# Kernel tuning notes

Hardware: AMD Instinct MI355X
Metric: run time of the kernel (lower is better)

## Reference

```python
import jax, jax.numpy as jnp
import numpy as np

N, E = 50000, 800000
IN_CH, OUT_CH, HEADS, EDGE_DIM = 128, 32, 4, 16
OUT_TOTAL = OUT_CH * HEADS  # 128 == IN_CH -> skip is Identity
NEG_SLOPE = 0.2
BN_EPS = 1e-5


def setup_inputs() -> dict:
    key = jax.random.key(0)
    ks = jax.random.split(key, 12)
    s = 1.0 / np.sqrt(IN_CH)
    return {
        "x": jax.random.normal(ks[0], (N, IN_CH), jnp.float32),
        "edge_index": jax.random.randint(ks[1], (2, E), 0, N, jnp.int64),
        "edge_attr": jax.random.normal(ks[2], (E, EDGE_DIM), jnp.float32),
        # GATv2Conv params (share_weights=False): lin_l, lin_r, lin_edge, att, bias
        "W_l": jax.random.uniform(ks[3], (IN_CH, OUT_TOTAL), jnp.float32, -s, s),
        "W_r": jax.random.uniform(ks[4], (IN_CH, OUT_TOTAL), jnp.float32, -s, s),
        "W_e": jax.random.uniform(ks[5], (EDGE_DIM, OUT_TOTAL), jnp.float32, -0.25, 0.25),
        "att": jax.random.uniform(ks[6], (HEADS, OUT_CH), jnp.float32, -s, s),
        "bias": jnp.zeros((OUT_TOTAL,), jnp.float32),
        "bn_gamma": jnp.ones((OUT_TOTAL,), jnp.float32),
        "bn_beta": jnp.zeros((OUT_TOTAL,), jnp.float32),
    }


def reference(x, edge_index, edge_attr, W_l, W_r, W_e, att, bias, bn_gamma, bn_beta):
    src, dst = edge_index[0], edge_index[1]
    # GATv2Conv: per-node linear projections, reshaped to [N, H, C]
    xl = (x @ W_l).reshape(N, HEADS, OUT_CH)
    xr = (x @ W_r).reshape(N, HEADS, OUT_CH)
    # edge-wise attention input: x_l[src] + x_r[dst] + lin_edge(edge_attr)
    e = xl[src] + xr[dst] + (edge_attr @ W_e).reshape(E, HEADS, OUT_CH)
    e = jax.nn.leaky_relu(e, NEG_SLOPE)
    score = jnp.einsum('ehc,hc->eh', e, att)  # [E, H]
    # segment softmax over destination nodes
    smax = jax.ops.segment_max(score, dst, num_segments=N)
    ex = jnp.exp(score - smax[dst])
    denom = jax.ops.segment_sum(ex, dst, num_segments=N)
    alpha = ex / denom[dst]  # [E, H]
    # weighted scatter-aggregation of source features
    msg = xl[src] * alpha[:, :, None]  # [E, H, C]
    out = jax.ops.segment_sum(msg, dst, num_segments=N).reshape(N, OUT_TOTAL) + bias
    # BatchNorm1d (training-mode batch stats, biased variance)
    mu = out.mean(axis=0)
    var = out.var(axis=0)
    out = (out - mu) * jax.lax.rsqrt(var + BN_EPS) * bn_gamma + bn_beta
    out = jax.nn.elu(out)
    # dropout: eval -> identity; skip: Identity (in_channels == out_total)
    return out + x
```

## Files before the change

### kernel.cpp

```cpp
#include <hip/hip_runtime.h>
#include <math.h>

#define N_NODES 50000
#define E_EDGES 800000
#define NEG_SLOPE 0.2f
#define BN_EPS 1e-5f
#define NB_SCAN 196
#define NWAVES 8192
#define LDB 132

using bf4 = __attribute__((ext_vector_type(4))) short;
using bf8 = __attribute__((ext_vector_type(8))) short;
using f32x4 = __attribute__((ext_vector_type(4))) float;

__device__ __forceinline__ unsigned short f2b(float f) {
  unsigned u = __float_as_uint(f);
  return (unsigned short)((u + 0x7FFFu + ((u >> 16) & 1u)) >> 16);
}

__global__ __launch_bounds__(256) void k_projm(
    const float* __restrict__ x, const float* __restrict__ Wl,
    const float* __restrict__ Wr, unsigned short* __restrict__ xlb,
    float* __restrict__ xr) {
  __shared__ __align__(16) unsigned short blds[256 * LDB];
  const int t = threadIdx.x;

#pragma unroll
  for (int s = 0; s < 32; ++s) {
    int i4 = s * 256 + t;
    int k = (i4 * 4) >> 8;
    int colb = (i4 * 4) & 255;
    float4 w = (colb < 128) ? *(const float4*)(Wl + k * 128 + colb)
                            : *(const float4*)(Wr + k * 128 + (colb - 128));
    blds[(colb + 0) * LDB + k] = f2b(w.x);
    blds[(colb + 1) * LDB + k] = f2b(w.y);
    blds[(colb + 2) * LDB + k] = f2b(w.z);
    blds[(colb + 3) * LDB + k] = f2b(w.w);
  }
  __syncthreads();

  const int wave = t >> 6, lane = t & 63;
  const int f = lane & 15;
  const int g = lane >> 4;
  const int r0 = blockIdx.x * 64 + wave * 16;
  const int row = r0 + f;
  const bool rok = row < N_NODES;

  f32x4 acc[16];
#pragma unroll
  for (int c = 0; c < 16; ++c) acc[c] = (f32x4){0.f, 0.f, 0.f, 0.f};

#pragma unroll
  for (int ks = 0; ks < 4; ++ks) {
    bf8 a;
    if (rok) {
      const float* ap = x + (size_t)row * 128 + ks * 32 + g * 8;
      float4 a0 = *(const float4*)(ap);
      float4 a1 = *(const float4*)(ap + 4);
      a = (bf8){(short)f2b(a0.x), (short)f2b(a0.y), (short)f2b(a0.z),
                (short)f2b(a0.w), (short)f2b(a1.x), (short)f2b(a1.y),
                (short)f2b(a1.z), (short)f2b(a1.w)};
    } else {
      a = (bf8){0, 0, 0, 0, 0, 0, 0, 0};
    }
#pragma unroll
    for (int c = 0; c < 16; ++c) {
      const bf4* bp =
          (const bf4*)(blds + (c * 16 + f) * LDB + ks * 32 + g * 8);
      bf8 b = __builtin_shufflevector(bp[0], bp[1], 0, 1, 2, 3, 4, 5, 6, 7);
      acc[c] = __builtin_amdgcn_mfma_f32_16x16x32_bf16(a, b, acc[c], 0, 0, 0);
    }
  }

#pragma unroll
  for (int c = 0; c < 16; ++c) {
    int cc = (c * 16 + f) & 127;
#pragma unroll
    for (int r = 0; r < 4; ++r) {
      int rr = r0 + g * 4 + r;
      if (rr < N_NODES) {
        if (c < 8)
          xlb[(size_t)rr * 128 + cc] = f2b(acc[c][r]);
        else
          xr[(size_t)rr * 128 + cc] = acc[c][r];
      }
    }
  }
}

__global__ __launch_bounds__(256) void k_count(const int* __restrict__ ei,
                                               int* __restrict__ deg) {
  int e = blockIdx.x * 256 + threadIdx.x;
  if (e < E_EDGES) atomicAdd(&deg[ei[E_EDGES + e]], 1);
}

__global__ __launch_bounds__(256) void k_scan_blk(const int* __restrict__ deg,
                                                  int* __restrict__ offs,
                                                  int* __restrict__ bsum) {
  __shared__ int s[256];
  int t = threadIdx.x, idx = blockIdx.x * 256 + t;
  int v = (idx < N_NODES) ? deg[idx] : 0;
  s[t] = v;
  __syncthreads();
  int acc = v;
#pragma unroll
  for (int off = 1; off < 256; off <<= 1) {
    int u = (t >= off) ? s[t - off] : 0;
    __syncthreads();
    acc += u;
    s[t] = acc;
    __syncthreads();
  }
  if (idx < N_NODES) offs[idx] = acc - v;
  if (t == 255) bsum[blockIdx.x] = acc;
}

__global__ __launch_bounds__(256) void k_scan_top(int* __restrict__ bsum) {
  __shared__ int s[256];
  int t = threadIdx.x;
  int v = (t < NB_SCAN) ? bsum[t] : 0;
  s[t] = v;
  __syncthreads();
  int acc = v;
#pragma unroll
  for (int off = 1; off < 256; off <<= 1) {
    int u = (t >= off) ? s[t - off] : 0;
    __syncthreads();
    acc += u;
    s[t] = acc;
    __syncthreads();
  }
  if (t < NB_SCAN) bsum[t] = acc - v;
}

__global__ __launch_bounds__(256) void k_scan_add(int* __restrict__ offs,
                                                  const int* __restrict__ bsum) {
  int idx = blockIdx.x * 256 + threadIdx.x;
  if (idx < N_NODES) offs[idx] += bsum[blockIdx.x];
}

__global__ __launch_bounds__(256) void k_fill(const int* __restrict__ ei,
                                              const int* __restrict__ offs,
                                              int* __restrict__ cur,
                                              int2* __restrict__ se) {
  int e = blockIdx.x * 256 + threadIdx.x;
  if (e >= E_EDGES) return;
  int d = ei[E_EDGES + e];
  int p = offs[d] + atomicAdd(&cur[d], 1);
  se[p] = make_int2(ei[e], e);
}

__device__ __forceinline__ float fscore(const float* __restrict__ ea, int e,
                                        const float* we0, const float* we1,
                                        float xrx, float xry, float ax,
                                        float ay, float xlx, float xly) {
  const float4* ea4 = (const float4*)(ea + (size_t)e * 16);
  float xe0 = 0.f, xe1 = 0.f;
#pragma unroll
  for (int k = 0; k < 4; ++k) {
    float4 v = ea4[k];
    xe0 += v.x * we0[4 * k] + v.y * we0[4 * k + 1] + v.z * we0[4 * k + 2] +
           v.w * we0[4 * k + 3];
    xe1 += v.x * we1[4 * k] + v.y * we1[4 * k + 1] + v.z * we1[4 * k + 2] +
           v.w * we1[4 * k + 3];
  }
  float v0 = xlx + xrx + xe0;
  float v1 = xly + xry + xe1;
  v0 = v0 > 0.f ? v0 : NEG_SLOPE * v0;
  v1 = v1 > 0.f ? v1 : NEG_SLOPE * v1;
  float p = v0 * ax + v1 * ay;
  p += __shfl_xor(p, 1);
  p += __shfl_xor(p, 2);
  p += __shfl_xor(p, 4);
  p += __shfl_xor(p, 8);
  return p;
}

#define UPD(p, xx, xy)              \
  {                                 \
    float mn = fmaxf(m, (p));       \
    float sc = __expf(m - mn);      \
    float pe = __expf((p)-mn);      \
    den = den * sc + pe;            \
    a0 = a0 * sc + pe * (xx);       \
    a1 = a1 * sc + pe * (xy);       \
    m = mn;                         \
  }

__global__ __launch_bounds__(256, 8) void k_node(
    const unsigned short* __restrict__ xlb, const float* __restrict__ xr,
    const int2* __restrict__ se, const float* __restrict__ ea,
    const float* __restrict__ We, const float* __restrict__ att,
    const int* __restrict__ offs, const int* __restrict__ deg,
    float* __restrict__ out) {
  const int wid =
      __builtin_amdgcn_readfirstlane((int)((blockIdx.x * 256 + threadIdx.x) >> 6));
  const int lane = threadIdx.x & 63;
  const int c0 = lane * 2;

  float we0[16], we1[16];
#pragma unroll
  for (int k = 0; k < 16; ++k) {
    float2 wv = *(const float2*)(We + k * 128 + c0);
    we0[k] = wv.x;
    we1[k] = wv.y;
  }
  float2 aw = *(const float2*)(att + c0);

  for (int d = wid; d < N_NODES; d += NWAVES) {
    const int base = __builtin_amdgcn_readfirstlane(offs[d]);
    const int n = __builtin_amdgcn_readfirstlane(deg[d]);
    float2 xrd = *(const float2*)(xr + (size_t)d * 128 + c0);

    float m = -INFINITY, den = 0.f, a0 = 0.f, a1 = 0.f;
    int i = 0;
    for (; i + 2 <= n; i += 2) {
      int2 q0 = se[base + i];
      int2 q1 = se[base + i + 1];
      int s0 = __builtin_amdgcn_readfirstlane(q0.x);
      int s1 = __builtin_amdgcn_readfirstlane(q1.x);
      int e0 = __builtin_amdgcn_readfirstlane(q0.y);
      int e1 = __builtin_amdgcn_readfirstlane(q1.y);
      unsigned uA = *(const unsigned*)(xlb + (size_t)s0 * 128 + c0);
      unsigned uB = *(const unsigned*)(xlb + (size_t)s1 * 128 + c0);
      float xAx = __uint_as_float(uA << 16);
      float xAy = __uint_as_float(uA & 0xFFFF0000u);
      float xBx = __uint_as_float(uB << 16);
      float xBy = __uint_as_float(uB & 0xFFFF0000u);
      float pA = fscore(ea, e0, we0, we1, xrd.x, xrd.y, aw.x, aw.y, xAx, xAy);
      float pB = fscore(ea, e1, we0, we1, xrd.x, xrd.y, aw.x, aw.y, xBx, xBy);
      UPD(pA, xAx, xAy);
      UPD(pB, xBx, xBy);
    }
    if (i < n) {
      int2 q = se[base + i];
      int s0 = __builtin_amdgcn_readfirstlane(q.x);
      int e0 = __builtin_amdgcn_readfirstlane(q.y);
      unsigned u = *(const unsigned*)(xlb + (size_t)s0 * 128 + c0);
      float xx = __uint_as_float(u << 16);
      float xy = __uint_as_float(u & 0xFFFF0000u);
      float p = fscore(ea, e0, we0, we1, xrd.x, xrd.y, aw.x, aw.y, xx, xy);
      UPD(p, xx, xy);
    }

    float inv = (n > 0) ? 1.f / den : 0.f;
    float2 o;
    o.x = a0 * inv;
    o.y = a1 * inv;
    *(float2*)(out + (size_t)d * 128 + c0) = o;
  }
}

__global__ __launch_bounds__(256) void k_bnstat(const float* __restrict__ out,
                                                float* __restrict__ bnsum,
                                                float* __restrict__ bnsq) {
  __shared__ float ls[256][4];
  __shared__ float lq[256][4];
  int t = threadIdx.x;
  int cg = t & 31;
  int rg = t >> 5;
  float s0 = 0, s1 = 0, s2 = 0, s3 = 0, q0 = 0, q1 = 0, q2 = 0, q3 = 0;
  for (int r = blockIdx.x * 8 + rg; r < N_NODES; r += gridDim.x * 8) {
    float4 v = ((const float4*)out)[(size_t)r * 32 + cg];
    s0 += v.x; s1 += v.y; s2 += v.z; s3 += v.w;
    q0 += v.x * v.x; q1 += v.y * v.y; q2 += v.z * v.z; q3 += v.w * v.w;
  }
  ls[t][0] = s0; ls[t][1] = s1; ls[t][2] = s2; ls[t][3] = s3;
  lq[t][0] = q0; lq[t][1] = q1; lq[t][2] = q2; lq[t][3] = q3;
  __syncthreads();
  if (t < 32) {
#pragma unroll
    for (int g = 1; g < 8; ++g) {
#pragma unroll
      for (int i = 0; i < 4; ++i) {
        ls[t][i] += ls[g * 32 + t][i];
        lq[t][i] += lq[g * 32 + t][i];
      }
    }
#pragma unroll
    for (int i = 0; i < 4; ++i) {
      unsafeAtomicAdd(bnsum + 4 * t + i, ls[t][i]);
      unsafeAtomicAdd(bnsq + 4 * t + i, lq[t][i]);
    }
  }
}

__global__ void k_bnparam(const float* __restrict__ bnsum,
                          const float* __restrict__ bnsq,
                          const float* __restrict__ gamma,
                          const float* __restrict__ beta,
                          float* __restrict__ scale, float* __restrict__ shift) {
  int j = threadIdx.x;
  float mu = bnsum[j] * (1.0f / N_NODES);
  float var = bnsq[j] * (1.0f / N_NODES) - mu * mu;
  float sc = gamma[j] * rsqrtf(var + BN_EPS);
  scale[j] = sc;
  shift[j] = beta[j] - mu * sc;
}

__global__ __launch_bounds__(256) void k_final(
    const float* __restrict__ agg, const float* __restrict__ x,
    const float* __restrict__ scale, const float* __restrict__ shift,
    float* __restrict__ out) {
  int i4 = blockIdx.x * 256 + threadIdx.x;
  if (i4 >= N_NODES * 128 / 4) return;
  int cbase = (i4 * 4) & 127;
  float4 v = ((const float4*)agg)[i4];
  float4 xv = ((const float4*)x)[i4];
  float4 sc = *(const float4*)(scale + cbase);
  float4 sh = *(const float4*)(shift + cbase);
  float r0 = v.x * sc.x + sh.x;
  float r1 = v.y * sc.y + sh.y;
  float r2 = v.z * sc.z + sh.z;
  float r3 = v.w * sc.w + sh.w;
  r0 = r0 > 0.f ? r0 : expm1f(r0);
  r1 = r1 > 0.f ? r1 : expm1f(r1);
  r2 = r2 > 0.f ? r2 : expm1f(r2);
  r3 = r3 > 0.f ? r3 : expm1f(r3);
  float4 o;
  o.x = r0 + xv.x; o.y = r1 + xv.y; o.z = r2 + xv.z; o.w = r3 + xv.w;
  ((float4*)out)[i4] = o;
}

extern "C" void kernel_launch(void* const* d_in, const int* in_sizes, int n_in,
                              void* d_out, int out_size, void* d_ws,
                              size_t ws_size, hipStream_t stream) {
  const float* x = (const float*)d_in[0];
  const int* ei = (const int*)d_in[1];
  const float* ea = (const float*)d_in[2];
  const float* Wl = (const float*)d_in[3];
  const float* Wr = (const float*)d_in[4];
  const float* We = (const float*)d_in[5];
  const float* att = (const float*)d_in[6];
  const float* gamma = (const float*)d_in[8];
  const float* beta = (const float*)d_in[9];
  float* out = (float*)d_out;

  unsigned short* xlb = (unsigned short*)d_ws;
  float* xr = (float*)(xlb + (size_t)N_NODES * 128);
  int* deg = (int*)(xr + (size_t)N_NODES * 128);
  int* offs = deg + N_NODES;
  int* cur = offs + N_NODES;
  int* bsum = cur + N_NODES;
  int2* se = (int2*)(bsum + 256);
  float* bnsum = (float*)(se + E_EDGES);
  float* bnsq = bnsum + 128;
  float* scale = bnsq + 128;
  float* shift = scale + 128;

  hipMemsetAsync(deg, 0, N_NODES * sizeof(int), stream);
  hipMemsetAsync(cur, 0, N_NODES * sizeof(int), stream);
  hipMemsetAsync(bnsum, 0, 2 * 128 * sizeof(float), stream);

  k_projm<<<(N_NODES + 63) / 64, 256, 0, stream>>>(x, Wl, Wr, xlb, xr);
  k_count<<<(E_EDGES + 255) / 256, 256, 0, stream>>>(ei, deg);
  k_scan_blk<<<NB_SCAN, 256, 0, stream>>>(deg, offs, bsum);
  k_scan_top<<<1, 256, 0, stream>>>(bsum);
  k_scan_add<<<NB_SCAN, 256, 0, stream>>>(offs, bsum);
  k_fill<<<(E_EDGES + 255) / 256, 256, 0, stream>>>(ei, offs, cur, se);
  k_node<<<NWAVES / 4, 256, 0, stream>>>(xlb, xr, se, ea, We, att, offs, deg,
                                         out);
  k_bnstat<<<256, 256, 0, stream>>>(out, bnsum, bnsq);
  k_bnparam<<<1, 128, 0, stream>>>(bnsum, bnsq, gamma, beta, scale, shift);
  k_final<<<(N_NODES * 128 / 4 + 255) / 256, 256, 0, stream>>>(out, x, scale,
                                                               shift, out);
}
```

Before: 282.6 us.

## Pre-sort fp16 edge attributes by destination, store xr in bf16, cut launches

The fill kernel now writes edge attributes in destination-sorted order as packed fp16, so the node kernel reads them contiguously instead of gathering fp32 rows by edge id. It computes the edge projection with fdot2, and xr is stored in bf16. Three memsets are folded into the projection and count kernels, the three-pass scan becomes one single-block kernel, and the BN parameter kernel is merged into the final kernel. This cuts launch count and gather traffic, at the cost of fp16/bf16 precision loss and extra writes in the fill kernel. The single-block serial scan and the zeroing of deg and cur inside k_projm rely on stream ordering before k_count.

After: 341.8 us. +21.0%, slower.

```diff
diff --git a/kernel.cpp b/kernel.cpp
--- a/kernel.cpp
+++ b/kernel.cpp
@@ -5,26 +5,38 @@
 #define E_EDGES 800000
 #define NEG_SLOPE 0.2f
 #define BN_EPS 1e-5f
-#define NB_SCAN 196
 #define NWAVES 8192
 #define LDB 132
+#define SCAN_T 1024
+#define SCAN_C 49
 
 using bf4 = __attribute__((ext_vector_type(4))) short;
 using bf8 = __attribute__((ext_vector_type(8))) short;
 using f32x4 = __attribute__((ext_vector_type(4))) float;
+using half2v = __attribute__((ext_vector_type(2))) _Float16;
 
 __device__ __forceinline__ unsigned short f2b(float f) {
   unsigned u = __float_as_uint(f);
   return (unsigned short)((u + 0x7FFFu + ((u >> 16) & 1u)) >> 16);
 }
+__device__ __forceinline__ float b2f_lo(unsigned u) {
+  return __uint_as_float(u << 16);
+}
+__device__ __forceinline__ float b2f_hi(unsigned u) {
+  return __uint_as_float(u & 0xFFFF0000u);
+}
 
 __global__ __launch_bounds__(256) void k_projm(
     const float* __restrict__ x, const float* __restrict__ Wl,
     const float* __restrict__ Wr, unsigned short* __restrict__ xlb,
-    float* __restrict__ xr) {
+    unsigned short* __restrict__ xrb, int* __restrict__ deg,
+    int* __restrict__ cur) {
+  const int t = threadIdx.x;
+  int gid = blockIdx.x * 256 + t;
+  if (gid < N_NODES) deg[gid] = 0;
+  else if (gid < 2 * N_NODES) cur[gid - N_NODES] = 0;
+
   __shared__ __align__(16) unsigned short blds[256 * LDB];
-  const int t = threadIdx.x;
-
 #pragma unroll
   for (int s = 0; s < 32; ++s) {
     int i4 = s * 256 + t;
@@ -74,95 +86,101 @@
 
 #pragma unroll
   for (int c = 0; c < 16; ++c) {
+    unsigned short* dst = (c < 8) ? xlb : xrb;
     int cc = (c * 16 + f) & 127;
 #pragma unroll
     for (int r = 0; r < 4; ++r) {
       int rr = r0 + g * 4 + r;
-      if (rr < N_NODES) {
-        if (c < 8)
-          xlb[(size_t)rr * 128 + cc] = f2b(acc[c][r]);
-        else
-          xr[(size_t)rr * 128 + cc] = acc[c][r];
-      }
+      if (rr < N_NODES) dst[(size_t)rr * 128 + cc] = f2b(acc[c][r]);
     }
   }
 }
 
 __global__ __launch_bounds__(256) void k_count(const int* __restrict__ ei,
-                                               int* __restrict__ deg) {
-  int e = blockIdx.x * 256 + threadIdx.x;
+                                               int* __restrict__ deg,
+                                               float* __restrict__ bn0) {
+  int t = threadIdx.x;
+  if (blockIdx.x == 0) bn0[t] = 0.f;
+  int e = blockIdx.x * 256 + t;
   if (e < E_EDGES) atomicAdd(&deg[ei[E_EDGES + e]], 1);
 }
 
-__global__ __launch_bounds__(256) void k_scan_blk(const int* __restrict__ deg,
-                                                  int* __restrict__ offs,
-                                                  int* __restrict__ bsum) {
-  __shared__ int s[256];
-  int t = threadIdx.x, idx = blockIdx.x * 256 + t;
-  int v = (idx < N_NODES) ? deg[idx] : 0;
-  s[t] = v;
+__global__ __launch_bounds__(SCAN_T) void k_scan(const int* __restrict__ deg,
+                                                 int* __restrict__ offs) {
+  __shared__ int ts[SCAN_T];
+  int t = threadIdx.x;
+  int base = t * SCAN_C;
+  int sum = 0;
+  for (int k = 0; k < SCAN_C; ++k) {
+    int idx = base + k;
+    if (idx < N_NODES) sum += deg[idx];
+  }
+  ts[t] = sum;
   __syncthreads();
-  int acc = v;
-#pragma unroll
-  for (int off = 1; off < 256; off <<= 1) {
-    int u = (t >= off) ? s[t - off] : 0;
+  int acc = sum;
+  for (int off = 1; off < SCAN_T; off <<= 1) {
+    int u = (t >= off) ? ts[t - off] : 0;
     __syncthreads();
     acc += u;
-    s[t] = acc;
+    ts[t] = acc;
     __syncthreads();
   }
-  if (idx < N_NODES) offs[idx] = acc - v;
-  if (t == 255) bsum[blockIdx.x] = acc;
-}
-
-__global__ __launch_bounds__(256) void k_scan_top(int* __restrict__ bsum) {
-  __shared__ int s[256];
-  int t = threadIdx.x;
-  int v = (t < NB_SCAN) ? bsum[t] : 0;
-  s[t] = v;
-  __syncthreads();
-  int acc = v;
-#pragma unroll
-  for (int off = 1; off < 256; off <<= 1) {
-    int u = (t >= off) ? s[t - off] : 0;
-    __syncthreads();
-    acc += u;
-    s[t] = acc;
-    __syncthreads();
-  }
-  if (t < NB_SCAN) bsum[t] = acc - v;
-}
-
-__global__ __launch_bounds__(256) void k_scan_add(int* __restrict__ offs,
-                                                  const int* __restrict__ bsum) {
-  int idx = blockIdx.x * 256 + threadIdx.x;
-  if (idx < N_NODES) offs[idx] += bsum[blockIdx.x];
+  int run = acc - sum;
+  for (int k = 0; k < SCAN_C; ++k) {
+    int idx = base + k;
+    if (idx < N_NODES) {
+      offs[idx] = run;
+      run += deg[idx];
+    }
+  }
 }
 
 __global__ __launch_bounds__(256) void k_fill(const int* __restrict__ ei,
+                                              const float* __restrict__ ea,
                                               const int* __restrict__ offs,
                                               int* __restrict__ cur,
-                                              int2* __restrict__ se) {
+                                              int* __restrict__ src_s,
+                                              int4* __restrict__ eah) {
   int e = blockIdx.x * 256 + threadIdx.x;
   if (e >= E_EDGES) return;
   int d = ei[E_EDGES + e];
   int p = offs[d] + atomicAdd(&cur[d], 1);
-  se[p] = make_int2(ei[e], e);
-}
-
-__device__ __forceinline__ float fscore(const float* __restrict__ ea, int e,
-                                        const float* we0, const float* we1,
-                                        float xrx, float xry, float ax,
-                                        float ay, float xlx, float xly) {
-  const float4* ea4 = (const float4*)(ea + (size_t)e * 16);
+  src_s[p] = ei[e];
+  const float4* r = (const float4*)(ea + (size_t)e * 16);
+  float4 v0 = r[0], v1 = r[1], v2 = r[2], v3 = r[3];
+  union {
+    half2v h[8];
+    int4 q[2];
+  } u;
+  u.h[0] = (half2v){(_Float16)v0.x, (_Float16)v0.y};
+  u.h[1] = (half2v){(_Float16)v0.z, (_Float16)v0.w};
+  u.h[2] = (half2v){(_Float16)v1.x, (_Float16)v1.y};
+  u.h[3] = (half2v){(_Float16)v1.z, (_Float16)v1.w};
+  u.h[4] = (half2v){(_Float16)v2.x, (_Float16)v2.y};
+  u.h[5] = (half2v){(_Float16)v2.z, (_Float16)v2.w};
+  u.h[6] = (half2v){(_Float16)v3.x, (_Float16)v3.y};
+  u.h[7] = (half2v){(_Float16)v3.z, (_Float16)v3.w};
+  eah[(size_t)p * 2] = u.q[0];
+  eah[(size_t)p * 2 + 1] = u.q[1];
+}
+
+__device__ __forceinline__ float fscore16(const half2v* eav,
+                                          const half2v* we0h,
+                                          const half2v* we1h, float xrx,
+                                          float xry, float ax, float ay,
+                                          float xlx, float xly) {
   float xe0 = 0.f, xe1 = 0.f;
 #pragma unroll
-  for (int k = 0; k < 4; ++k) {
-    float4 v = ea4[k];
-    xe0 += v.x * we0[4 * k] + v.y * we0[4 * k + 1] + v.z * we0[4 * k + 2] +
-           v.w * we0[4 * k + 3];
-    xe1 += v.x * we1[4 * k] + v.y * we1[4 * k + 1] + v.z * we1[4 * k + 2] +
-           v.w * we1[4 * k + 3];
+  for (int k = 0; k < 8; ++k) {
+#if __has_builtin(__builtin_amdgcn_fdot2)
+    xe0 = __builtin_amdgcn_fdot2(eav[k], we0h[k], xe0, false);
+    xe1 = __builtin_amdgcn_fdot2(eav[k], we1h[k], xe1, false);
+#else
+    xe0 += (float)eav[k][0] * (float)we0h[k][0] +
+           (float)eav[k][1] * (float)we0h[k][1];
+    xe1 += (float)eav[k][0] * (float)we1h[k][0] +
+           (float)eav[k][1] * (float)we1h[k][1];
+#endif
   }
   float v0 = xlx + xrx + xe0;
   float v1 = xly + xry + xe1;
@@ -188,58 +206,67 @@
   }
 
 __global__ __launch_bounds__(256, 8) void k_node(
-    const unsigned short* __restrict__ xlb, const float* __restrict__ xr,
-    const int2* __restrict__ se, const float* __restrict__ ea,
-    const float* __restrict__ We, const float* __restrict__ att,
-    const int* __restrict__ offs, const int* __restrict__ deg,
-    float* __restrict__ out) {
-  const int wid =
-      __builtin_amdgcn_readfirstlane((int)((blockIdx.x * 256 + threadIdx.x) >> 6));
+    const unsigned short* __restrict__ xlb,
+    const unsigned short* __restrict__ xrb, const int* __restrict__ src_s,
+    const int4* __restrict__ eah, const float* __restrict__ We,
+    const float* __restrict__ att, const int* __restrict__ offs,
+    const int* __restrict__ deg, float* __restrict__ out) {
+  const int wid = __builtin_amdgcn_readfirstlane(
+      (int)((blockIdx.x * 256 + threadIdx.x) >> 6));
   const int lane = threadIdx.x & 63;
   const int c0 = lane * 2;
 
-  float we0[16], we1[16];
-#pragma unroll
-  for (int k = 0; k < 16; ++k) {
-    float2 wv = *(const float2*)(We + k * 128 + c0);
-    we0[k] = wv.x;
-    we1[k] = wv.y;
+  half2v we0h[8], we1h[8];
+#pragma unroll
+  for (int j = 0; j < 8; ++j) {
+    float2 wa = *(const float2*)(We + (2 * j) * 128 + c0);
+    float2 wb = *(const float2*)(We + (2 * j + 1) * 128 + c0);
+    we0h[j] = (half2v){(_Float16)wa.x, (_Float16)wb.x};
+    we1h[j] = (half2v){(_Float16)wa.y, (_Float16)wb.y};
   }
   float2 aw = *(const float2*)(att + c0);
 
   for (int d = wid; d < N_NODES; d += NWAVES) {
     const int base = __builtin_amdgcn_readfirstlane(offs[d]);
     const int n = __builtin_amdgcn_readfirstlane(deg[d]);
-    float2 xrd = *(const float2*)(xr + (size_t)d * 128 + c0);
+    unsigned ur = *(const unsigned*)(xrb + (size_t)d * 128 + c0);
+    float xrx = b2f_lo(ur), xry = b2f_hi(ur);
 
     float m = -INFINITY, den = 0.f, a0 = 0.f, a1 = 0.f;
     int i = 0;
     for (; i + 2 <= n; i += 2) {
-      int2 q0 = se[base + i];
-      int2 q1 = se[base + i + 1];
-      int s0 = __builtin_amdgcn_readfirstlane(q0.x);
-      int s1 = __builtin_amdgcn_readfirstlane(q1.x);
-      int e0 = __builtin_amdgcn_readfirstlane(q0.y);
-      int e1 = __builtin_amdgcn_readfirstlane(q1.y);
+      int s0 = __builtin_amdgcn_readfirstlane(src_s[base + i]);
+      int s1 = __builtin_amdgcn_readfirstlane(src_s[base + i + 1]);
+      union {
+        int4 q[4];
+        half2v h[16];
+      } u;
+      u.q[0] = eah[(size_t)(base + i) * 2];
+      u.q[1] = eah[(size_t)(base + i) * 2 + 1];
+      u.q[2] = eah[(size_t)(base + i) * 2 + 2];
+      u.q[3] = eah[(size_t)(base + i) * 2 + 3];
       unsigned uA = *(const unsigned*)(xlb + (size_t)s0 * 128 + c0);
       unsigned uB = *(const unsigned*)(xlb + (size_t)s1 * 128 + c0);
-      float xAx = __uint_as_float(uA << 16);
-      float xAy = __uint_as_float(uA & 0xFFFF0000u);
-      float xBx = __uint_as_float(uB << 16);
-      float xBy = __uint_as_float(uB & 0xFFFF0000u);
-      float pA = fscore(ea, e0, we0, we1, xrd.x, xrd.y, aw.x, aw.y, xAx, xAy);
-      float pB = fscore(ea, e1, we0, we1, xrd.x, xrd.y, aw.x, aw.y, xBx, xBy);
+      float xAx = b2f_lo(uA), xAy = b2f_hi(uA);
+      float xBx = b2f_lo(uB), xBy = b2f_hi(uB);
+      float pA =
+          fscore16(u.h, we0h, we1h, xrx, xry, aw.x, aw.y, xAx, xAy);
+      float pB =
+          fscore16(u.h + 8, we0h, we1h, xrx, xry, aw.x, aw.y, xBx, xBy);
       UPD(pA, xAx, xAy);
       UPD(pB, xBx, xBy);
     }
     if (i < n) {
-      int2 q = se[base + i];
-      int s0 = __builtin_amdgcn_readfirstlane(q.x);
-      int e0 = __builtin_amdgcn_readfirstlane(q.y);
-      unsigned u = *(const unsigned*)(xlb + (size_t)s0 * 128 + c0);
-      float xx = __uint_as_float(u << 16);
-      float xy = __uint_as_float(u & 0xFFFF0000u);
-      float p = fscore(ea, e0, we0, we1, xrd.x, xrd.y, aw.x, aw.y, xx, xy);
+      int s0 = __builtin_amdgcn_readfirstlane(src_s[base + i]);
+      union {
+        int4 q[2];
+        half2v h[8];
+      } u;
+      u.q[0] = eah[(size_t)(base + i) * 2];
+      u.q[1] = eah[(size_t)(base + i) * 2 + 1];
+      unsigned uv = *(const unsigned*)(xlb + (size_t)s0 * 128 + c0);
+      float xx = b2f_lo(uv), xy = b2f_hi(uv);
+      float p = fscore16(u.h, we0h, we1h, xrx, xry, aw.x, aw.y, xx, xy);
       UPD(p, xx, xy);
     }
 
@@ -285,30 +312,29 @@
   }
 }
 
-__global__ void k_bnparam(const float* __restrict__ bnsum,
-                          const float* __restrict__ bnsq,
-                          const float* __restrict__ gamma,
-                          const float* __restrict__ beta,
-                          float* __restrict__ scale, float* __restrict__ shift) {
-  int j = threadIdx.x;
-  float mu = bnsum[j] * (1.0f / N_NODES);
-  float var = bnsq[j] * (1.0f / N_NODES) - mu * mu;
-  float sc = gamma[j] * rsqrtf(var + BN_EPS);
-  scale[j] = sc;
-  shift[j] = beta[j] - mu * sc;
-}
-
 __global__ __launch_bounds__(256) void k_final(
     const float* __restrict__ agg, const float* __restrict__ x,
-    const float* __restrict__ scale, const float* __restrict__ shift,
+    const float* __restrict__ bnsum, const float* __restrict__ bnsq,
+    const float* __restrict__ gamma, const float* __restrict__ beta,
     float* __restrict__ out) {
-  int i4 = blockIdx.x * 256 + threadIdx.x;
-  if (i4 >= N_NODES * 128 / 4) return;
+  __shared__ __align__(16) float ssc[128];
+  __shared__ __align__(16) float ssh[128];
+  int t = threadIdx.x;
+  if (t < 128) {
+    float mu = bnsum[t] * (1.0f / N_NODES);
+    float var = bnsq[t] * (1.0f / N_NODES) - mu * mu;
+    float sc = gamma[t] * rsqrtf(var + BN_EPS);
+    ssc[t] = sc;
+    ssh[t] = beta[t] - mu * sc;
+  }
+  __syncthreads();
+  int i4 = blockIdx.x * 256 + t;
+  if (i4 >= N_NODES * 32) return;
   int cbase = (i4 * 4) & 127;
   float4 v = ((const float4*)agg)[i4];
   float4 xv = ((const float4*)x)[i4];
-  float4 sc = *(const float4*)(scale + cbase);
-  float4 sh = *(const float4*)(shift + cbase);
+  float4 sc = *(const float4*)(ssc + cbase);
+  float4 sh = *(const float4*)(ssh + cbase);
   float r0 = v.x * sc.x + sh.x;
   float r1 = v.y * sc.y + sh.y;
   float r2 = v.z * sc.z + sh.z;
@@ -337,31 +363,24 @@
   float* out = (float*)d_out;
 
   unsigned short* xlb = (unsigned short*)d_ws;
-  float* xr = (float*)(xlb + (size_t)N_NODES * 128);
-  int* deg = (int*)(xr + (size_t)N_NODES * 128);
+  unsigned short* xrb = xlb + (size_t)N_NODES * 128;
+  int* deg = (int*)(xrb + (size_t)N_NODES * 128);
   int* offs = deg + N_NODES;
   int* cur = offs + N_NODES;
-  int* bsum = cur + N_NODES;
-  int2* se = (int2*)(bsum + 256);
-  float* bnsum = (float*)(se + E_EDGES);
+  int* src_s = cur + N_NODES;
+  int4* eah = (int4*)(src_s + E_EDGES);
+  float* bnsum = (float*)(eah + (size_t)E_EDGES * 2);
   float* bnsq = bnsum + 128;
-  float* scale = bnsq + 128;
-  float* shift = scale + 128;
-
-  hipMemsetAsync(deg, 0, N_NODES * sizeof(int), stream);
-  hipMemsetAsync(cur, 0, N_NODES * sizeof(int), stream);
-  hipMemsetAsync(bnsum, 0, 2 * 128 * sizeof(float), stream);
-
-  k_projm<<<(N_NODES + 63) / 64, 256, 0, stream>>>(x, Wl, Wr, xlb, xr);
-  k_count<<<(E_EDGES + 255) / 256, 256, 0, stream>>>(ei, deg);
-  k_scan_blk<<<NB_SCAN, 256, 0, stream>>>(deg, offs, bsum);
-  k_scan_top<<<1, 256, 0, stream>>>(bsum);
-  k_scan_add<<<NB_SCAN, 256, 0, stream>>>(offs, bsum);
-  k_fill<<<(E_EDGES + 255) / 256, 256, 0, stream>>>(ei, offs, cur, se);
-  k_node<<<NWAVES / 4, 256, 0, stream>>>(xlb, xr, se, ea, We, att, offs, deg,
-                                         out);
+
+  k_projm<<<(N_NODES + 63) / 64, 256, 0, stream>>>(x, Wl, Wr, xlb, xrb, deg,
+                                                   cur);
+  k_count<<<(E_EDGES + 255) / 256, 256, 0, stream>>>(ei, deg, bnsum);
+  k_scan<<<1, SCAN_T, 0, stream>>>(deg, offs);
+  k_fill<<<(E_EDGES + 255) / 256, 256, 0, stream>>>(ei, ea, offs, cur, src_s,
+                                                    eah);
+  k_node<<<NWAVES / 4, 256, 0, stream>>>(xlb, xrb, src_s, eah, We, att, offs,
+                                         deg, out);
   k_bnstat<<<256, 256, 0, stream>>>(out, bnsum, bnsq);
-  k_bnparam<<<1, 128, 0, stream>>>(bnsum, bnsq, gamma, beta, scale, shift);
-  k_final<<<(N_NODES * 128 / 4 + 255) / 256, 256, 0, stream>>>(out, x, scale,
-                                                               shift, out);
-}
+  k_final<<<(N_NODES * 32 + 255) / 256, 256, 0, stream>>>(out, x, bnsum, bnsq,
+                                                          gamma, beta, out);
+}
```
